# Optimization experiments

Measured on AMD Instinct MI355X. Metric: run time of the kernel, lower is better.

The kernel has to match this reference:

```python
import jax, jax.numpy as jnp
import numpy as np
jax.config.update("jax_enable_x64", True)

N, VDIM, D = 65536, 3, 256
EPS = 1e-3


def setup_inputs() -> dict:
    key = jax.random.key(0)
    k1, _ = jax.random.split(key)
    inp = jax.random.normal(k1, (N, VDIM, D), dtype=jnp.float32)
    weight = jnp.ones((D,), dtype=jnp.float32)
    return {"input": inp, "weight": weight}


def _symsqrtinv(covar, eps):
    # covar: (N, 3, 3) symmetric PSD (fp64). Matches torch .svd() semantics.
    u, s, vt = jnp.linalg.svd(covar)
    v = jnp.swapaxes(vt, -1, -2)  # torch.svd returns V, jnp returns V^T
    thresh = s.max(-1, keepdims=True) * s.shape[-1] * jnp.finfo(s.dtype).eps
    good = s > thresh
    inv = jnp.where(good, 1.0 / jnp.sqrt(s + eps), 0.0)  # drop bad components
    return (v * inv[..., None, :]) @ vt  # V diag(inv) V^T


def reference(input, weight):
    x = input.astype(jnp.float64)
    x = x - x.mean(-1, keepdims=True)                      # mean-center over width d
    reg = jnp.diag(jnp.asarray([1.0, 2.0, 3.0], dtype=x.dtype))
    covar = (x @ jnp.swapaxes(x, -1, -2)) / D + EPS * reg  # (N, 3, 3)
    covar_sqrtinv = _symsqrtinv(covar, EPS)
    out = (covar_sqrtinv @ x).astype(weight.dtype) * weight.reshape(1, 1, D)
    return out
```

## Files before the change

### kernel.cpp

```cpp
#include <hip/hip_runtime.h>


namespace {

constexpr int kD = 256;
constexpr float kEps = 1e-3f;
constexpr int kNSIters = 8;

__device__ __forceinline__ void symmul(const float* M, const float* N, float* P) {
    P[0] = M[0]*N[0] + M[1]*N[1] + M[2]*N[2];
    P[1] = M[0]*N[1] + M[1]*N[3] + M[2]*N[4];
    P[2] = M[0]*N[2] + M[1]*N[4] + M[2]*N[5];
    P[3] = M[1]*N[1] + M[3]*N[3] + M[4]*N[4];
    P[4] = M[1]*N[2] + M[3]*N[4] + M[4]*N[5];
    P[5] = M[2]*N[2] + M[4]*N[4] + M[5]*N[5];
}

__global__ __launch_bounds__(256) void eqln_kernel(const float* __restrict__ in,
                                                   const float* __restrict__ wptr,
                                                   float* __restrict__ out,
                                                   int nrows) {
    const int lane = threadIdx.x & 63;
    const int row  = blockIdx.x * (blockDim.x >> 6) + (threadIdx.x >> 6);
    if (row >= nrows) return;

    const size_t base = (size_t)row * (3 * kD);
    const int col = lane * 4;

    const float4 x0 = *(const float4*)(in + base + 0 * kD + col);
    const float4 x1 = *(const float4*)(in + base + 1 * kD + col);
    const float4 x2 = *(const float4*)(in + base + 2 * kD + col);
    const float4 w  = *(const float4*)(wptr + col);

    float s[9];
    s[0] = x0.x + x0.y + x0.z + x0.w;
    s[1] = x1.x + x1.y + x1.z + x1.w;
    s[2] = x2.x + x2.y + x2.z + x2.w;
    s[3] = x0.x*x0.x + x0.y*x0.y + x0.z*x0.z + x0.w*x0.w;
    s[4] = x0.x*x1.x + x0.y*x1.y + x0.z*x1.z + x0.w*x1.w;
    s[5] = x0.x*x2.x + x0.y*x2.y + x0.z*x2.z + x0.w*x2.w;
    s[6] = x1.x*x1.x + x1.y*x1.y + x1.z*x1.z + x1.w*x1.w;
    s[7] = x1.x*x2.x + x1.y*x2.y + x1.z*x2.z + x1.w*x2.w;
    s[8] = x2.x*x2.x + x2.y*x2.y + x2.z*x2.z + x2.w*x2.w;

    #pragma unroll
    for (int off = 32; off > 0; off >>= 1) {
        #pragma unroll
        for (int i = 0; i < 9; ++i) s[i] += __shfl_xor(s[i], off, 64);
    }

    const float inv_d = 1.0f / (float)kD;
    const float m0 = s[0] * inv_d, m1 = s[1] * inv_d, m2 = s[2] * inv_d;

    float B[6];
    B[0] = s[3] * inv_d - m0 * m0 + 2.0f * kEps;
    B[1] = s[4] * inv_d - m0 * m1;
    B[2] = s[5] * inv_d - m0 * m2;
    B[3] = s[6] * inv_d - m1 * m1 + 3.0f * kEps;
    B[4] = s[7] * inv_d - m1 * m2;
    B[5] = s[8] * inv_d - m2 * m2 + 4.0f * kEps;

    const float tr  = B[0] + B[3] + B[5];
    const float itr = 1.0f / tr;
    float Y[6] = {B[0]*itr, B[1]*itr, B[2]*itr, B[3]*itr, B[4]*itr, B[5]*itr};
    float Z[6] = {1.0f, 0.0f, 0.0f, 1.0f, 0.0f, 1.0f};

    #pragma unroll
    for (int it = 0; it < kNSIters; ++it) {
        float W[6], T[6], Yn[6], Zn[6];
        symmul(Z, Y, W);
        T[0] = 1.5f - 0.5f * W[0];
        T[1] = -0.5f * W[1];
        T[2] = -0.5f * W[2];
        T[3] = 1.5f - 0.5f * W[3];
        T[4] = -0.5f * W[4];
        T[5] = 1.5f - 0.5f * W[5];
        symmul(Y, T, Yn);
        symmul(T, Z, Zn);
        #pragma unroll
        for (int i = 0; i < 6; ++i) { Y[i] = Yn[i]; Z[i] = Zn[i]; }
    }

    const float sc  = 1.0f / sqrtf(tr);
    const float M00 = Z[0] * sc, M01 = Z[1] * sc, M02 = Z[2] * sc;
    const float M11 = Z[3] * sc, M12 = Z[4] * sc, M22 = Z[5] * sc;

    const float a0[4] = {x0.x - m0, x0.y - m0, x0.z - m0, x0.w - m0};
    const float a1[4] = {x1.x - m1, x1.y - m1, x1.z - m1, x1.w - m1};
    const float a2[4] = {x2.x - m2, x2.y - m2, x2.z - m2, x2.w - m2};
    const float wv[4] = {w.x, w.y, w.z, w.w};

    float r0[4], r1[4], r2[4];
    #pragma unroll
    for (int i = 0; i < 4; ++i) {
        r0[i] = (M00 * a0[i] + M01 * a1[i] + M02 * a2[i]) * wv[i];
        r1[i] = (M01 * a0[i] + M11 * a1[i] + M12 * a2[i]) * wv[i];
        r2[i] = (M02 * a0[i] + M12 * a1[i] + M22 * a2[i]) * wv[i];
    }

    *(float4*)(out + base + 0 * kD + col) = make_float4(r0[0], r0[1], r0[2], r0[3]);
    *(float4*)(out + base + 1 * kD + col) = make_float4(r1[0], r1[1], r1[2], r1[3]);
    *(float4*)(out + base + 2 * kD + col) = make_float4(r2[0], r2[1], r2[2], r2[3]);
}

}

extern "C" void kernel_launch(void* const* d_in, const int* in_sizes, int n_in,
                              void* d_out, int out_size, void* d_ws, size_t ws_size,
                              hipStream_t stream) {
    (void)n_in; (void)d_ws; (void)ws_size; (void)out_size;
    const float* in   = (const float*)d_in[0];
    const float* wght = (const float*)d_in[1];
    float* out = (float*)d_out;

    const int nrows = in_sizes[0] / (3 * kD);
    const int rows_per_block = 256 / 64;
    const int blocks = (nrows + rows_per_block - 1) / rows_per_block;

    eqln_kernel<<<blocks, 256, 0, stream>>>(in, wght, out, nrows);
}
```

Before: 338.4 us.

## Process each row with 16 lanes instead of a full wavefront

Each row is now handled by 16 threads, each holding 16 elements per channel, instead of 64 threads holding 4. The aim is to cut per-row redundant work: the shuffle reduction drops from 6 to 4 steps and the serial Newton-Schulz iteration runs on 4x fewer threads. In exchange each thread uses more registers, and each wave now serves four rows with loads strided in 256-byte chunks.

```diff
diff --git a/kernel.cpp b/kernel.cpp
--- a/kernel.cpp
+++ b/kernel.cpp
@@ -20,31 +20,37 @@
                                                    const float* __restrict__ wptr,
                                                    float* __restrict__ out,
                                                    int nrows) {
-    const int lane = threadIdx.x & 63;
-    const int row  = blockIdx.x * (blockDim.x >> 6) + (threadIdx.x >> 6);
+    const int tid     = threadIdx.x;
+    const int lane_in = tid & 15;
+    const int row     = blockIdx.x * (blockDim.x >> 4) + (tid >> 4);
     if (row >= nrows) return;
 
     const size_t base = (size_t)row * (3 * kD);
-    const int col = lane * 4;
+    const int coff = lane_in * 4;
 
-    const float4 x0 = *(const float4*)(in + base + 0 * kD + col);
-    const float4 x1 = *(const float4*)(in + base + 1 * kD + col);
-    const float4 x2 = *(const float4*)(in + base + 2 * kD + col);
-    const float4 w  = *(const float4*)(wptr + col);
+    float4 x[3][4];
+    #pragma unroll
+    for (int v = 0; v < 3; ++v)
+        #pragma unroll
+        for (int j = 0; j < 4; ++j)
+            x[v][j] = *(const float4*)(in + base + v * kD + j * 64 + coff);
 
-    float s[9];
-    s[0] = x0.x + x0.y + x0.z + x0.w;
-    s[1] = x1.x + x1.y + x1.z + x1.w;
-    s[2] = x2.x + x2.y + x2.z + x2.w;
-    s[3] = x0.x*x0.x + x0.y*x0.y + x0.z*x0.z + x0.w*x0.w;
-    s[4] = x0.x*x1.x + x0.y*x1.y + x0.z*x1.z + x0.w*x1.w;
-    s[5] = x0.x*x2.x + x0.y*x2.y + x0.z*x2.z + x0.w*x2.w;
-    s[6] = x1.x*x1.x + x1.y*x1.y + x1.z*x1.z + x1.w*x1.w;
-    s[7] = x1.x*x2.x + x1.y*x2.y + x1.z*x2.z + x1.w*x2.w;
-    s[8] = x2.x*x2.x + x2.y*x2.y + x2.z*x2.z + x2.w*x2.w;
+    float s[9] = {0.f, 0.f, 0.f, 0.f, 0.f, 0.f, 0.f, 0.f, 0.f};
+    #pragma unroll
+    for (int j = 0; j < 4; ++j) {
+        const float* a = (const float*)&x[0][j];
+        const float* b = (const float*)&x[1][j];
+        const float* c = (const float*)&x[2][j];
+        #pragma unroll
+        for (int k = 0; k < 4; ++k) {
+            s[0] += a[k];      s[1] += b[k];      s[2] += c[k];
+            s[3] += a[k]*a[k]; s[4] += a[k]*b[k]; s[5] += a[k]*c[k];
+            s[6] += b[k]*b[k]; s[7] += b[k]*c[k]; s[8] += c[k]*c[k];
+        }
+    }
 
     #pragma unroll
-    for (int off = 32; off > 0; off >>= 1) {
+    for (int off = 8; off > 0; off >>= 1) {
         #pragma unroll
         for (int i = 0; i < 9; ++i) s[i] += __shfl_xor(s[i], off, 64);
     }
@@ -85,22 +91,28 @@
     const float M00 = Z[0] * sc, M01 = Z[1] * sc, M02 = Z[2] * sc;
     const float M11 = Z[3] * sc, M12 = Z[4] * sc, M22 = Z[5] * sc;
 
-    const float a0[4] = {x0.x - m0, x0.y - m0, x0.z - m0, x0.w - m0};
-    const float a1[4] = {x1.x - m1, x1.y - m1, x1.z - m1, x1.w - m1};
-    const float a2[4] = {x2.x - m2, x2.y - m2, x2.z - m2, x2.w - m2};
-    const float wv[4] = {w.x, w.y, w.z, w.w};
-
-    float r0[4], r1[4], r2[4];
     #pragma unroll
-    for (int i = 0; i < 4; ++i) {
-        r0[i] = (M00 * a0[i] + M01 * a1[i] + M02 * a2[i]) * wv[i];
-        r1[i] = (M01 * a0[i] + M11 * a1[i] + M12 * a2[i]) * wv[i];
-        r2[i] = (M02 * a0[i] + M12 * a1[i] + M22 * a2[i]) * wv[i];
+    for (int j = 0; j < 4; ++j) {
+        const float4 wv = *(const float4*)(wptr + j * 64 + coff);
+        const float* a  = (const float*)&x[0][j];
+        const float* b  = (const float*)&x[1][j];
+        const float* c  = (const float*)&x[2][j];
+        const float* w  = (const float*)&wv;
+        float4 r0, r1, r2;
+        float* p0 = (float*)&r0; float* p1 = (float*)&r1; float* p2 = (float*)&r2;
+        #pragma unroll
+        for (int k = 0; k < 4; ++k) {
+            const float a0 = a[k] - m0;
+            const float a1 = b[k] - m1;
+            const float a2 = c[k] - m2;
+            p0[k] = (M00 * a0 + M01 * a1 + M02 * a2) * w[k];
+            p1[k] = (M01 * a0 + M11 * a1 + M12 * a2) * w[k];
+            p2[k] = (M02 * a0 + M12 * a1 + M22 * a2) * w[k];
+        }
+        *(float4*)(out + base + 0 * kD + j * 64 + coff) = r0;
+        *(float4*)(out + base + 1 * kD + j * 64 + coff) = r1;
+        *(float4*)(out + base + 2 * kD + j * 64 + coff) = r2;
     }
-
-    *(float4*)(out + base + 0 * kD + col) = make_float4(r0[0], r0[1], r0[2], r0[3]);
-    *(float4*)(out + base + 1 * kD + col) = make_float4(r1[0], r1[1], r1[2], r1[3]);
-    *(float4*)(out + base + 2 * kD + col) = make_float4(r2[0], r2[1], r2[2], r2[3]);
 }
 
 }
@@ -114,7 +126,7 @@
     float* out = (float*)d_out;
 
     const int nrows = in_sizes[0] / (3 * kD);
-    const int rows_per_block = 256 / 64;
+    const int rows_per_block = 256 / 16;
     const int blocks = (nrows + rows_per_block - 1) / rows_per_block;
 
     eqln_kernel<<<blocks, 256, 0, stream>>>(in, wght, out, nrows);
```

Result: no change. 332.4 us (-1.8%).
